# Kernel optimization log

Measured on AMD Instinct MI355X. Metric: run time of the kernel, lower is better.

The kernel has to match this reference:

```python
import jax, jax.numpy as jnp
import numpy as np

QP = 127.0          # signed symmetric 8-bit: Qp = 2**(8-1)-1
MIN_RANGE = 1e-6


def _ste_round(q):
    # round_pass: straight-through estimator round
    return q + jax.lax.stop_gradient(jnp.round(q) - q)


def _quant_per_token(x):
    # symmetric per-token: amax over last dim, keepdim
    s = jnp.clip(jnp.max(jnp.abs(x), axis=-1, keepdims=True), MIN_RANGE, None) / QP
    return _ste_round(x / s), s


def _quant_per_tensor(w):
    s = jnp.clip(jnp.max(jnp.abs(w)), MIN_RANGE, None) / QP
    return _ste_round(w / s), s


def _qlinear(x2d, w, b):
    # fake-quant linear: quantize act per-token, weight per-tensor,
    # int-domain matmul, bias added before dequant rescale (faithful to source)
    qx, sx = _quant_per_token(x2d)      # [N,K], [N,1]
    qw, sw = _quant_per_tensor(w)       # [M,K], scalar
    out = jnp.matmul(qx, qw.T) + b[None, :]
    return out * (sx * sw)              # [N,M]


def setup_inputs() -> dict:
    key = jax.random.key(0)
    k1, k2, k3, k4, k5 = jax.random.split(key, 5)
    B, S, D, H = 64, 197, 768, 3072
    return {
        "x": jax.random.normal(k1, (B, S, D), dtype=jnp.float32),
        "w1": jax.random.normal(k2, (H, D), dtype=jnp.float32) * 0.02,
        "b1": jax.random.normal(k3, (H,), dtype=jnp.float32) * 0.02,
        "w2": jax.random.normal(k4, (D, H), dtype=jnp.float32) * 0.02,
        "b2": jax.random.normal(k5, (D,), dtype=jnp.float32) * 0.02,
    }


def reference(x, w1, b1, w2, b2):
    B, S, D = x.shape
    x2d = x.reshape(-1, D)                         # view(-1, x.size(-1))
    h = _qlinear(x2d, w1, b1)                      # fc1
    h = jax.nn.gelu(h, approximate=False)          # ViT Mlp activation (exact GELU)
    o = _qlinear(h, w2, b2)                        # fc2
    return o.reshape(B, S, -1)
```

## Files before the change

kernel.cpp:

```cpp
#include <hip/hip_runtime.h>
#include <stdint.h>

#define QPF  127.0f
#define MINR 1e-6f

typedef int v4i __attribute__((ext_vector_type(4)));

__device__ __forceinline__ float wave_max64(float v) {
  v = fmaxf(v, __shfl_xor(v, 32, 64));
  v = fmaxf(v, __shfl_xor(v, 16, 64));
  v = fmaxf(v, __shfl_xor(v, 8, 64));
  v = fmaxf(v, __shfl_xor(v, 4, 64));
  v = fmaxf(v, __shfl_xor(v, 2, 64));
  v = fmaxf(v, __shfl_xor(v, 1, 64));
  return v;
}

__device__ __forceinline__ float gelu_exact(float x) {
  float z = fabsf(x) * 0.70710678118654752440f;
  float t = __builtin_amdgcn_rcpf(fmaf(0.3275911f, z, 1.0f));
  float p = fmaf(fmaf(fmaf(fmaf(1.061405429f, t, -1.453152027f), t,
                           1.421413741f), t, -0.284496736f), t, 0.254829592f) * t;
  float e = __expf(-z * z);
  float erfz = fmaf(-p, e, 1.0f);
  float cdf = fmaf(0.5f, copysignf(erfz, x), 0.5f);
  return x * cdf;
}

__device__ __forceinline__ void gl2lds16(const void* g, void* l) {
  __builtin_amdgcn_global_load_lds(
      (const __attribute__((address_space(1))) int*)g,
      (__attribute__((address_space(3))) int*)l,
      16, 0, 0);
}

__global__ __launch_bounds__(256) void amax_kernel(const float* __restrict__ w,
                                                   int n4, unsigned* out) {
  const float4* w4 = (const float4*)w;
  float m = 0.f;
  for (int i = blockIdx.x * blockDim.x + threadIdx.x; i < n4;
       i += gridDim.x * blockDim.x) {
    float4 v = w4[i];
    m = fmaxf(m, fmaxf(fmaxf(fabsf(v.x), fabsf(v.y)),
                       fmaxf(fabsf(v.z), fabsf(v.w))));
  }
  m = wave_max64(m);
  __shared__ float red[4];
  const int lane = threadIdx.x & 63, wv = threadIdx.x >> 6;
  if (lane == 0) red[wv] = m;
  __syncthreads();
  if (threadIdx.x == 0) {
    float mm = fmaxf(fmaxf(red[0], red[1]), fmaxf(red[2], red[3]));
    atomicMax(out, __float_as_uint(mm));
  }
}

__global__ __launch_bounds__(256) void wquant_kernel(const float* __restrict__ w,
                                                     int n4,
                                                     const unsigned* __restrict__ amaxbits,
                                                     signed char* __restrict__ q) {
  const float s = fmaxf(__uint_as_float(*amaxbits), MINR) / QPF;
  const float rs = 1.0f / s;
  const float4* w4 = (const float4*)w;
  char4* q4 = (char4*)q;
  for (int i = blockIdx.x * blockDim.x + threadIdx.x; i < n4;
       i += gridDim.x * blockDim.x) {
    float4 v = w4[i];
    char4 c;
    c.x = (signed char)(int)rintf(v.x * rs);
    c.y = (signed char)(int)rintf(v.y * rs);
    c.z = (signed char)(int)rintf(v.z * rs);
    c.w = (signed char)(int)rintf(v.w * rs);
    q4[i] = c;
  }
}

__global__ __launch_bounds__(256) void xquant_kernel(const float* __restrict__ x,
                                                     signed char* __restrict__ qx,
                                                     float* __restrict__ sx, int K) {
  const int token = blockIdx.x;
  const float4* xr = (const float4*)(x + (size_t)token * K);
  const int k4 = K >> 2;
  float m = 0.f;
  for (int i = threadIdx.x; i < k4; i += 256) {
    float4 v = xr[i];
    m = fmaxf(m, fmaxf(fmaxf(fabsf(v.x), fabsf(v.y)),
                       fmaxf(fabsf(v.z), fabsf(v.w))));
  }
  m = wave_max64(m);
  __shared__ float red[4];
  const int lane = threadIdx.x & 63, wv = threadIdx.x >> 6;
  if (lane == 0) red[wv] = m;
  __syncthreads();
  const float M = fmaxf(fmaxf(red[0], red[1]), fmaxf(red[2], red[3]));
  const float s = fmaxf(M, MINR) / QPF;
  const float rs = 1.0f / s;
  if (threadIdx.x == 0) sx[token] = s;
  char4* qr = (char4*)(qx + (size_t)token * K);
  for (int i = threadIdx.x; i < k4; i += 256) {
    float4 v = xr[i];
    char4 c;
    c.x = (signed char)(int)rintf(v.x * rs);
    c.y = (signed char)(int)rintf(v.y * rs);
    c.z = (signed char)(int)rintf(v.z * rs);
    c.w = (signed char)(int)rintf(v.w * rs);
    qr[i] = c;
  }
}

__global__ __launch_bounds__(256) void hquant_kernel(const float* __restrict__ h,
                                                     const unsigned* __restrict__ amaxbits,
                                                     signed char* __restrict__ qh,
                                                     float* __restrict__ sh, int K) {
  const int token = blockIdx.x;
  const float s = fmaxf(__uint_as_float(amaxbits[token]), MINR) / QPF;
  const float rs = 1.0f / s;
  if (threadIdx.x == 0) sh[token] = s;
  const float4* hr = (const float4*)(h + (size_t)token * K);
  char4* qr = (char4*)(qh + (size_t)token * K);
  for (int i = threadIdx.x; i < (K >> 2); i += 256) {
    float4 v = hr[i];
    char4 c;
    c.x = (signed char)(int)rintf(v.x * rs);
    c.y = (signed char)(int)rintf(v.y * rs);
    c.z = (signed char)(int)rintf(v.z * rs);
    c.w = (signed char)(int)rintf(v.w * rs);
    qr[i] = c;
  }
}

template <bool GELU_EPI>
__global__ __launch_bounds__(256, 2) void gemm_i8(
    const signed char* __restrict__ A,
    const signed char* __restrict__ B,
    const float* __restrict__ bias,
    const float* __restrict__ sA,
    const unsigned* __restrict__ sBbits,
    float* __restrict__ out,
    unsigned* __restrict__ amax_out,
    int N, int K, int Mout) {
  __shared__ __align__(16) signed char As[128 * 64];
  __shared__ __align__(16) signed char Bs[128 * 64];

  const int t = threadIdx.x;
  const int lane = t & 63;
  const int wv = t >> 6;
  const int wm = wv >> 1;
  const int wn = wv & 1;
  const int rowBlk = blockIdx.y * 128;
  const int colBlk = blockIdx.x * 128;

  int ar0 = rowBlk + wv * 16 + (lane >> 2);
  int ar1 = ar0 + 64;
  if (ar0 > N - 1) ar0 = N - 1;
  if (ar1 > N - 1) ar1 = N - 1;
  const int br0 = colBlk + wv * 16 + (lane >> 2);
  const int br1 = br0 + 64;
  const int kb = (((lane & 3) ^ ((lane >> 3) & 3)) * 16);

  const signed char* gA0 = A + (size_t)ar0 * K + kb;
  const signed char* gA1 = A + (size_t)ar1 * K + kb;
  const signed char* gB0 = B + (size_t)br0 * K + kb;
  const signed char* gB1 = B + (size_t)br1 * K + kb;

  signed char* lA0 = As + wv * 1024;
  signed char* lA1 = As + 4096 + wv * 1024;
  signed char* lB0 = Bs + wv * 1024;
  signed char* lB1 = Bs + 4096 + wv * 1024;

  const v4i vzero = {0, 0, 0, 0};
  v4i acc[4][4];
#pragma unroll
  for (int i = 0; i < 4; i++)
#pragma unroll
    for (int j = 0; j < 4; j++) acc[i][j] = vzero;

  const int swz = ((lane >> 4) ^ ((lane >> 1) & 3)) * 16;
  const int aoff = (wm * 64 + (lane & 15)) * 64 + swz;
  const int boff = (wn * 64 + (lane & 15)) * 64 + swz;

  for (int kt = 0; kt < K; kt += 64) {
    gl2lds16(gA0, lA0);
    gl2lds16(gA1, lA1);
    gl2lds16(gB0, lB0);
    gl2lds16(gB1, lB1);
    __syncthreads();

    v4i a[4], b[4];
#pragma unroll
    for (int mi = 0; mi < 4; mi++) a[mi] = *(const v4i*)(As + aoff + mi * 1024);
#pragma unroll
    for (int ni = 0; ni < 4; ni++) b[ni] = *(const v4i*)(Bs + boff + ni * 1024);
#pragma unroll
    for (int mi = 0; mi < 4; mi++)
#pragma unroll
      for (int ni = 0; ni < 4; ni++)
        acc[mi][ni] = __builtin_amdgcn_mfma_i32_16x16x64_i8(a[mi], b[ni],
                                                            acc[mi][ni], 0, 0, 0);
    __syncthreads();
    gA0 += 64; gA1 += 64; gB0 += 64; gB1 += 64;
  }

  const float sB = fmaxf(__uint_as_float(*sBbits), MINR) / QPF;
  const int colb = colBlk + wn * 64 + (lane & 15);
  const int rowb = rowBlk + wm * 64 + (lane >> 4) * 4;

  float bv[4];
#pragma unroll
  for (int ni = 0; ni < 4; ni++) bv[ni] = bias[colb + ni * 16];

#pragma unroll
  for (int mi = 0; mi < 4; mi++) {
    const int row0 = rowb + mi * 16;
    float sAv[4];
#pragma unroll
    for (int r = 0; r < 4; r++) sAv[r] = (row0 + r < N) ? sA[row0 + r] : 0.f;
    float rmax[4] = {0.f, 0.f, 0.f, 0.f};
#pragma unroll
    for (int ni = 0; ni < 4; ni++) {
#pragma unroll
      for (int r = 0; r < 4; r++) {
        float v = ((float)acc[mi][ni][r] + bv[ni]) * (sAv[r] * sB);
        if (GELU_EPI) v = gelu_exact(v);
        rmax[r] = fmaxf(rmax[r], fabsf(v));
        if (row0 + r < N)
          out[(size_t)(row0 + r) * Mout + colb + ni * 16] = v;
      }
    }
    if (GELU_EPI) {
#pragma unroll
      for (int r = 0; r < 4; r++) {
        float m = rmax[r];
        m = fmaxf(m, __shfl_xor(m, 1, 64));
        m = fmaxf(m, __shfl_xor(m, 2, 64));
        m = fmaxf(m, __shfl_xor(m, 4, 64));
        m = fmaxf(m, __shfl_xor(m, 8, 64));
        if ((lane & 15) == 0 && row0 + r < N)
          atomicMax(amax_out + row0 + r, __float_as_uint(m));
      }
    }
  }
}

extern "C" void kernel_launch(void* const* d_in, const int* in_sizes, int n_in,
                              void* d_out, int out_size, void* d_ws, size_t ws_size,
                              hipStream_t stream) {
  const float* x  = (const float*)d_in[0];
  const float* w1 = (const float*)d_in[1];
  const float* b1 = (const float*)d_in[2];
  const float* w2 = (const float*)d_in[3];
  const float* b2 = (const float*)d_in[4];

  const int H = in_sizes[2];
  const int D = in_sizes[4];
  const int N = in_sizes[0] / D;
  float* out = (float*)d_out;

  char* ws = (char*)d_ws;
  auto alloc = [&](size_t bytes) {
    char* p = ws;
    ws += (bytes + 255) & ~(size_t)255;
    return p;
  };
  signed char* qx  = (signed char*)alloc((size_t)N * D);
  signed char* qw1 = (signed char*)alloc((size_t)H * D);
  signed char* qw2 = (signed char*)alloc((size_t)H * D);
  signed char* qh  = (signed char*)alloc((size_t)N * H);
  float*    sx     = (float*)alloc((size_t)N * 4);
  float*    sh     = (float*)alloc((size_t)N * 4);
  unsigned* amaxh  = (unsigned*)alloc((size_t)N * 4);
  unsigned* wamax  = (unsigned*)alloc(256);
  float*    h      = (float*)alloc((size_t)N * H * 4);
  (void)ws_size;

  hipMemsetAsync(amaxh, 0, (size_t)N * 4, stream);
  hipMemsetAsync(wamax, 0, 8, stream);

  const int n4w = (H * D) >> 2;
  amax_kernel<<<512, 256, 0, stream>>>(w1, n4w, wamax + 0);
  amax_kernel<<<512, 256, 0, stream>>>(w2, n4w, wamax + 1);
  wquant_kernel<<<1024, 256, 0, stream>>>(w1, n4w, wamax + 0, qw1);
  wquant_kernel<<<1024, 256, 0, stream>>>(w2, n4w, wamax + 1, qw2);
  xquant_kernel<<<N, 256, 0, stream>>>(x, qx, sx, D);

  dim3 g1(H / 128, (N + 127) / 128);
  gemm_i8<true><<<g1, 256, 0, stream>>>(qx, qw1, b1, sx, wamax + 0, h, amaxh,
                                        N, D, H);
  hquant_kernel<<<N, 256, 0, stream>>>(h, amaxh, qh, sh, H);

  dim3 g2(D / 128, (N + 127) / 128);
  gemm_i8<false><<<g2, 256, 0, stream>>>(qh, qw2, b2, sh, wamax + 1, out,
                                         nullptr, N, H, D);
}
```

Before: 284.1 us.

## Double-buffer GEMM LDS tiles and store GELU intermediate as fp16

The int8 GEMM main loop now uses two LDS buffers: the next K-tile is prefetched while MFMAs run on the current one, and the trailing barrier is dropped. Separately, the fc1 GELU output is written in fp16 instead of fp32, which halves the intermediate traffic read back by the h-quantization kernel. The risk is that fp16 rounding of h before requantization can flip some int8 roundings relative to the fp32 reference, and the doubled LDS (32 KB per block) may limit occupancy.

```diff
diff --git a/kernel.cpp b/kernel.cpp
--- a/kernel.cpp
+++ b/kernel.cpp
@@ -5,6 +5,8 @@
 #define MINR 1e-6f
 
 typedef int v4i __attribute__((ext_vector_type(4)));
+typedef _Float16 h8 __attribute__((ext_vector_type(8)));
+typedef signed char c8 __attribute__((ext_vector_type(8)));
 
 __device__ __forceinline__ float wave_max64(float v) {
   v = fmaxf(v, __shfl_xor(v, 32, 64));
@@ -108,7 +110,7 @@
   }
 }
 
-__global__ __launch_bounds__(256) void hquant_kernel(const float* __restrict__ h,
+__global__ __launch_bounds__(256) void hquant_kernel(const _Float16* __restrict__ h,
                                                      const unsigned* __restrict__ amaxbits,
                                                      signed char* __restrict__ qh,
                                                      float* __restrict__ sh, int K) {
@@ -116,15 +118,14 @@
   const float s = fmaxf(__uint_as_float(amaxbits[token]), MINR) / QPF;
   const float rs = 1.0f / s;
   if (threadIdx.x == 0) sh[token] = s;
-  const float4* hr = (const float4*)(h + (size_t)token * K);
-  char4* qr = (char4*)(qh + (size_t)token * K);
-  for (int i = threadIdx.x; i < (K >> 2); i += 256) {
-    float4 v = hr[i];
-    char4 c;
-    c.x = (signed char)(int)rintf(v.x * rs);
-    c.y = (signed char)(int)rintf(v.y * rs);
-    c.z = (signed char)(int)rintf(v.z * rs);
-    c.w = (signed char)(int)rintf(v.w * rs);
+  const h8* hr = (const h8*)(h + (size_t)token * K);
+  c8* qr = (c8*)(qh + (size_t)token * K);
+  for (int i = threadIdx.x; i < (K >> 3); i += 256) {
+    h8 v = hr[i];
+    c8 c;
+#pragma unroll
+    for (int j = 0; j < 8; j++)
+      c[j] = (signed char)(int)rintf((float)v[j] * rs);
     qr[i] = c;
   }
 }
@@ -136,11 +137,11 @@
     const float* __restrict__ bias,
     const float* __restrict__ sA,
     const unsigned* __restrict__ sBbits,
-    float* __restrict__ out,
+    void* __restrict__ outv,
     unsigned* __restrict__ amax_out,
     int N, int K, int Mout) {
-  __shared__ __align__(16) signed char As[128 * 64];
-  __shared__ __align__(16) signed char Bs[128 * 64];
+  __shared__ __align__(16) signed char As[2 * 128 * 64];
+  __shared__ __align__(16) signed char Bs[2 * 128 * 64];
 
   const int t = threadIdx.x;
   const int lane = t & 63;
@@ -163,11 +164,6 @@
   const signed char* gB0 = B + (size_t)br0 * K + kb;
   const signed char* gB1 = B + (size_t)br1 * K + kb;
 
-  signed char* lA0 = As + wv * 1024;
-  signed char* lA1 = As + 4096 + wv * 1024;
-  signed char* lB0 = Bs + wv * 1024;
-  signed char* lB1 = Bs + 4096 + wv * 1024;
-
   const v4i vzero = {0, 0, 0, 0};
   v4i acc[4][4];
 #pragma unroll
@@ -179,26 +175,44 @@
   const int aoff = (wm * 64 + (lane & 15)) * 64 + swz;
   const int boff = (wn * 64 + (lane & 15)) * 64 + swz;
 
-  for (int kt = 0; kt < K; kt += 64) {
-    gl2lds16(gA0, lA0);
-    gl2lds16(gA1, lA1);
-    gl2lds16(gB0, lB0);
-    gl2lds16(gB1, lB1);
+  const int T = K >> 6;
+
+  {
+    signed char* a = As + wv * 1024;
+    signed char* b = Bs + wv * 1024;
+    gl2lds16(gA0, a);
+    gl2lds16(gA1, a + 4096);
+    gl2lds16(gB0, b);
+    gl2lds16(gB1, b + 4096);
+    gA0 += 64; gA1 += 64; gB0 += 64; gB1 += 64;
+  }
+
+  int buf = 0;
+  for (int kt = 0; kt < T; ++kt) {
     __syncthreads();
-
+    if (kt + 1 < T) {
+      const int o = (buf ^ 1) * 8192;
+      signed char* a = As + o + wv * 1024;
+      signed char* b = Bs + o + wv * 1024;
+      gl2lds16(gA0, a);
+      gl2lds16(gA1, a + 4096);
+      gl2lds16(gB0, b);
+      gl2lds16(gB1, b + 4096);
+      gA0 += 64; gA1 += 64; gB0 += 64; gB1 += 64;
+    }
+    const int o = buf * 8192;
     v4i a[4], b[4];
 #pragma unroll
-    for (int mi = 0; mi < 4; mi++) a[mi] = *(const v4i*)(As + aoff + mi * 1024);
-#pragma unroll
-    for (int ni = 0; ni < 4; ni++) b[ni] = *(const v4i*)(Bs + boff + ni * 1024);
+    for (int mi = 0; mi < 4; mi++) a[mi] = *(const v4i*)(As + o + aoff + mi * 1024);
+#pragma unroll
+    for (int ni = 0; ni < 4; ni++) b[ni] = *(const v4i*)(Bs + o + boff + ni * 1024);
 #pragma unroll
     for (int mi = 0; mi < 4; mi++)
 #pragma unroll
       for (int ni = 0; ni < 4; ni++)
         acc[mi][ni] = __builtin_amdgcn_mfma_i32_16x16x64_i8(a[mi], b[ni],
                                                             acc[mi][ni], 0, 0, 0);
-    __syncthreads();
-    gA0 += 64; gA1 += 64; gB0 += 64; gB1 += 64;
+    buf ^= 1;
   }
 
   const float sB = fmaxf(__uint_as_float(*sBbits), MINR) / QPF;
@@ -223,8 +237,13 @@
         float v = ((float)acc[mi][ni][r] + bv[ni]) * (sAv[r] * sB);
         if (GELU_EPI) v = gelu_exact(v);
         rmax[r] = fmaxf(rmax[r], fabsf(v));
-        if (row0 + r < N)
-          out[(size_t)(row0 + r) * Mout + colb + ni * 16] = v;
+        if (row0 + r < N) {
+          const size_t idx = (size_t)(row0 + r) * Mout + colb + ni * 16;
+          if (GELU_EPI)
+            ((_Float16*)outv)[idx] = (_Float16)v;
+          else
+            ((float*)outv)[idx] = v;
+        }
       }
     }
     if (GELU_EPI) {
@@ -270,7 +289,7 @@
   float*    sh     = (float*)alloc((size_t)N * 4);
   unsigned* amaxh  = (unsigned*)alloc((size_t)N * 4);
   unsigned* wamax  = (unsigned*)alloc(256);
-  float*    h      = (float*)alloc((size_t)N * H * 4);
+  _Float16* h      = (_Float16*)alloc((size_t)N * H * 2);
   (void)ws_size;
 
   hipMemsetAsync(amaxh, 0, (size_t)N * 4, stream);
@@ -284,11 +303,11 @@
   xquant_kernel<<<N, 256, 0, stream>>>(x, qx, sx, D);
 
   dim3 g1(H / 128, (N + 127) / 128);
-  gemm_i8<true><<<g1, 256, 0, stream>>>(qx, qw1, b1, sx, wamax + 0, h, amaxh,
-                                        N, D, H);
+  gemm_i8<true><<<g1, 256, 0, stream>>>(qx, qw1, b1, sx, wamax + 0, (void*)h,
+                                        amaxh, N, D, H);
   hquant_kernel<<<N, 256, 0, stream>>>(h, amaxh, qh, sh, H);
 
   dim3 g2(D / 128, (N + 127) / 128);
-  gemm_i8<false><<<g2, 256, 0, stream>>>(qh, qw2, b2, sh, wamax + 1, out,
+  gemm_i8<false><<<g2, 256, 0, stream>>>(qh, qw2, b2, sh, wamax + 1, (void*)out,
                                          nullptr, N, H, D);
 }
```

New measurement: 272.3 us. 1.04x faster.
